# Performance work log

Hardware: AMD Instinct MI355X
Metric: run time of the kernel (lower is better)

The kernel has to match this reference:

```python
import jax, jax.numpy as jnp
from jax import lax
import numpy as np

B, T, I, H, OUT = 4096, 168, 4, 64, 12


def setup_inputs() -> dict:
    key = jax.random.key(0)
    ks = jax.random.split(key, 14)
    s = 0.05
    return {
        "x": jax.random.normal(ks[0], (B, T, I), dtype=jnp.float32),
        # LSTM layer 0 (PyTorch gate order: i, f, g, o)
        "Wih0": jax.random.normal(ks[1], (4 * H, I), dtype=jnp.float32) * s,
        "Whh0": jax.random.normal(ks[2], (4 * H, H), dtype=jnp.float32) * s,
        "bih0": jax.random.normal(ks[3], (4 * H,), dtype=jnp.float32) * s,
        "bhh0": jax.random.normal(ks[4], (4 * H,), dtype=jnp.float32) * s,
        # LSTM layer 1
        "Wih1": jax.random.normal(ks[5], (4 * H, H), dtype=jnp.float32) * s,
        "Whh1": jax.random.normal(ks[6], (4 * H, H), dtype=jnp.float32) * s,
        "bih1": jax.random.normal(ks[7], (4 * H,), dtype=jnp.float32) * s,
        "bhh1": jax.random.normal(ks[8], (4 * H,), dtype=jnp.float32) * s,
        # FC head: Linear(64,64) -> ReLU -> Linear(64,12)
        "W1": jax.random.normal(ks[9], (64, H), dtype=jnp.float32) * s,
        "b1": jax.random.normal(ks[10], (64,), dtype=jnp.float32) * s,
        "W2": jax.random.normal(ks[11], (OUT, 64), dtype=jnp.float32) * s,
        "b2": jax.random.normal(ks[12], (OUT,), dtype=jnp.float32) * s,
    }


def _lstm_layer(x, Wih, Whh, bih, bhh):
    # x: [B, T, in]; returns hidden sequence [B, T, H]
    Bsz = x.shape[0]
    Hd = Whh.shape[1]
    # Precompute input contribution for all timesteps: [B, T, 4H]
    xg = jnp.einsum('bti,gi->btg', x, Wih) + bih + bhh

    def step(carry, xg_t):
        h, c = carry
        g = xg_t + h @ Whh.T  # [B, 4H]
        i, f, gg, o = jnp.split(g, 4, axis=-1)
        i = jax.nn.sigmoid(i)
        f = jax.nn.sigmoid(f)
        gg = jnp.tanh(gg)
        o = jax.nn.sigmoid(o)
        c = f * c + i * gg
        h = o * jnp.tanh(c)
        return (h, c), h

    h0 = jnp.zeros((Bsz, Hd), x.dtype)
    (_, _), hs = lax.scan(step, (h0, h0), jnp.swapaxes(xg, 0, 1))  # hs: [T, B, H]
    return jnp.swapaxes(hs, 0, 1)


def reference(x, Wih0, Whh0, bih0, bhh0, Wih1, Whh1, bih1, bhh1, W1, b1, W2, b2):
    # Eval-mode forward: dropout layers are identity.
    h1 = _lstm_layer(x, Wih0, Whh0, bih0, bhh0)   # [B, T, H]
    h2 = _lstm_layer(h1, Wih1, Whh1, bih1, bhh1)  # [B, T, H]
    last = h2[:, -1, :]                            # [B, H]
    z = jax.nn.relu(last @ W1.T + b1)              # [B, 64]
    out = z @ W2.T + b2                            # [B, 12]
    return out.reshape(-1, 3, 4)
```

## Files before the change

### kernel.cpp

```cpp
#include <hip/hip_runtime.h>


typedef _Float16 h8 __attribute__((ext_vector_type(8)));
typedef _Float16 h4 __attribute__((ext_vector_type(4)));
typedef float f4 __attribute__((ext_vector_type(4)));

#define ROWB 208
#define HBUF (16 * ROWB)
#define H0_OFF 0
#define H1_OFF (2 * HBUF)
#define SMEM_TOTAL (4 * HBUF)

#define K1F 1.4426950408889634f
#define K2F 2.8853900817779268f

__device__ __forceinline__ float exp2_(float x) {
#if __has_builtin(__builtin_amdgcn_exp2f)
  return __builtin_amdgcn_exp2f(x);
#else
  float r; asm("v_exp_f32 %0, %1" : "=v"(r) : "v"(x)); return r;
#endif
}
__device__ __forceinline__ float rcp_(float x) {
#if __has_builtin(__builtin_amdgcn_rcpf)
  return __builtin_amdgcn_rcpf(x);
#else
  float r; asm("v_rcp_f32 %0, %1" : "=v"(r) : "v"(x)); return r;
#endif
}

__device__ __forceinline__ f4 mfma16(h8 a, h8 b, f4 c) {
  return __builtin_amdgcn_mfma_f32_16x16x32_f16(a, b, c, 0, 0, 0);
}

__device__ __forceinline__ h8 load_w8s(const float* __restrict__ p, float sc) {
  h8 r;
#pragma unroll
  for (int j = 0; j < 8; j++) r[j] = (_Float16)(p[j] * sc);
  return r;
}

__device__ __forceinline__ void lstm_act_s(float gi, float gf, float gg, float go,
                                           float& c, float& h) {
  float Ei = exp2_(-gi);
  float Ef = exp2_(-gf);
  float Eg = exp2_(gg);
  float Eo = exp2_(-go);
  float A = 1.f + Ei, B = 1.f + Ef, C = 1.f + Eg, D = 1.f + Eo;
  float AB = A * B, CD = C * D, BD = B * D;
  float R  = rcp_(AB * CD);
  float fv = (A * CD) * R;
  float ig = (BD * (Eg - 1.f)) * R;
  float ov = (AB * C) * R;
  c = fv * c + ig;
  float r2 = rcp_(exp2_(c * K2F) + 1.f);
  h = ov * (1.f - 2.f * r2);
}

extern "C" __global__ void __launch_bounds__(512, 2)
weather_lstm_mfma12(const float* __restrict__ x,
                    const float* __restrict__ Wih0, const float* __restrict__ Whh0,
                    const float* __restrict__ bih0, const float* __restrict__ bhh0,
                    const float* __restrict__ Wih1, const float* __restrict__ Whh1,
                    const float* __restrict__ bih1, const float* __restrict__ bhh1,
                    const float* __restrict__ W1, const float* __restrict__ b1,
                    const float* __restrict__ W2, const float* __restrict__ b2,
                    float* __restrict__ out)
{
  __shared__ __align__(16) unsigned char smem[SMEM_TOTAL];
  const int tid  = threadIdx.x;
  const int lane = tid & 63;
  const int w    = tid >> 6;
  const int col  = lane & 15;
  const int quad = lane >> 4;
  const int role = (w ^ (w >> 2)) & 1;
  const bool isL0 = (role == 0);
  const int adj  = (w >= 4) ? ((w & 1) ? -1 : 1) : 0;
  const int wl   = (w + adj) >> 1;
  const int u0   = wl * 16;
  const int uu   = u0 + quad * 4;
  const int sB   = blockIdx.x * 16;

  h8 wfrag[16];
  f4 bias[4];
#pragma unroll
  for (int g = 0; g < 4; ++g) {
    const float sc = (g == 2) ? K2F : K1F;
    const int r = g * 64 + u0 + col;
    if (isL0) {
#pragma unroll
      for (int f = 0; f < 2; ++f)
        wfrag[2 * g + f] = load_w8s(Whh0 + r * 64 + f * 32 + quad * 8, sc);
      h8 xw = {};
      if (quad == 0) {
#pragma unroll
        for (int j = 0; j < 4; ++j) xw[j] = (_Float16)(Wih0[r * 4 + j] * sc);
      }
      wfrag[8 + g] = xw;
#pragma unroll
      for (int j = 0; j < 4; ++j)
        bias[g][j] = (bih0[g * 64 + uu + j] + bhh0[g * 64 + uu + j]) * sc;
    } else {
#pragma unroll
      for (int f = 0; f < 2; ++f) {
        wfrag[2 * g + f]     = load_w8s(Wih1 + r * 64 + f * 32 + quad * 8, sc);
        wfrag[8 + 2 * g + f] = load_w8s(Whh1 + r * 64 + f * 32 + quad * 8, sc);
      }
#pragma unroll
      for (int j = 0; j < 4; ++j)
        bias[g][j] = (bih1[g * 64 + uu + j] + bhh1[g * 64 + uu + j]) * sc;
    }
  }

  for (int idx = tid; idx < SMEM_TOTAL / 4; idx += 512) ((int*)smem)[idx] = 0;
  __syncthreads();

  f4 xc = {};
  if (isL0 && quad == 0)
    xc = *(const f4*)(x + ((size_t)(sB + col) * 168 + 0) * 4);

  f4 acc[4];
  float cst[4] = {0.f, 0.f, 0.f, 0.f};
  float hl[4]  = {0.f, 0.f, 0.f, 0.f};
  const int bo = col * ROWB + quad * 16;
  const int wo = col * ROWB + uu * 2;

  for (int k = 0; k <= 169; ++k) {
    const int sl = k & 1, slp = sl ^ 1;

    if (isL0) {
      if (k <= 167) {
        const unsigned char* h0r = smem + H0_OFF + slp * HBUF;
        h8 b0  = *(const h8*)(h0r + bo);
        h8 b1v = *(const h8*)(h0r + bo + 64);
        h8 bx = {};
        if (quad == 0) {
#pragma unroll
          for (int j = 0; j < 4; ++j) bx[j] = (_Float16)xc[j];
        }
        {
          const int kn = (k < 167) ? k + 1 : k;
          f4 xn = xc;
          if (quad == 0)
            xn = *(const f4*)(x + ((size_t)(sB + col) * 168 + kn) * 4);
          xc = xn;
        }
#pragma unroll
        for (int g = 0; g < 4; ++g) acc[g] = mfma16(wfrag[2 * g], b0, bias[g]);
#pragma unroll
        for (int g = 0; g < 4; ++g) acc[g] = mfma16(wfrag[2 * g + 1], b1v, acc[g]);
#pragma unroll
        for (int g = 0; g < 4; ++g) acc[g] = mfma16(wfrag[8 + g], bx, acc[g]);
      }
    } else {
      if (k >= 2) {
        h4 hv;
#pragma unroll
        for (int a = 0; a < 4; ++a) {
          float ho;
          lstm_act_s(acc[0][a], acc[1][a], acc[2][a], acc[3][a], cst[a], ho);
          hl[a] = ho;
          hv[a] = (_Float16)ho;
        }
        *(h4*)(smem + H1_OFF + sl * HBUF + wo) = hv;
      }
    }
    __syncthreads();

    if (isL0) {
      if (k <= 167) {
        h4 hv;
#pragma unroll
        for (int a = 0; a < 4; ++a) {
          float ho;
          lstm_act_s(acc[0][a], acc[1][a], acc[2][a], acc[3][a], cst[a], ho);
          hv[a] = (_Float16)ho;
        }
        *(h4*)(smem + H0_OFF + sl * HBUF + wo) = hv;
      }
    } else {
      if (k >= 1 && k <= 168) {
        const unsigned char* h0r = smem + H0_OFF + slp * HBUF;
        const unsigned char* h1r = smem + H1_OFF + sl * HBUF;
        h8 b0  = *(const h8*)(h0r + bo);
        h8 b1v = *(const h8*)(h0r + bo + 64);
        h8 q0  = *(const h8*)(h1r + bo);
        h8 q1  = *(const h8*)(h1r + bo + 64);
#pragma unroll
        for (int g = 0; g < 4; ++g) acc[g] = mfma16(wfrag[2 * g], b0, bias[g]);
#pragma unroll
        for (int g = 0; g < 4; ++g) acc[g] = mfma16(wfrag[2 * g + 1], b1v, acc[g]);
#pragma unroll
        for (int g = 0; g < 4; ++g) acc[g] = mfma16(wfrag[8 + 2 * g], q0, acc[g]);
#pragma unroll
        for (int g = 0; g < 4; ++g) acc[g] = mfma16(wfrag[9 + 2 * g], q1, acc[g]);
      }
    }
    __syncthreads();
  }

  float* fh = (float*)smem;
  if (!isL0) {
    f4 hv; hv[0] = hl[0]; hv[1] = hl[1]; hv[2] = hl[2]; hv[3] = hl[3];
    *(f4*)(fh + col * 64 + uu) = hv;
  }
  __syncthreads();

  {
    const int u = tid & 63, g2 = tid >> 6;
    const float* w1r = W1 + u * 64;
    float* zl = (float*)(smem + 4096);
#pragma unroll
    for (int rep = 0; rep < 2; ++rep) {
      const int s2 = g2 + rep * 8;
      float za = b1[u];
      const float* f0 = fh + s2 * 64;
      for (int j = 0; j < 64; ++j) za += w1r[j] * f0[j];
      zl[s2 * 64 + u] = fmaxf(za, 0.f);
    }
  }
  __syncthreads();

  if (tid < 192) {
    const float* zl = (const float*)(smem + 4096);
    const int s2 = tid / 12, o = tid - s2 * 12;
    float a = b2[o];
    for (int j = 0; j < 64; ++j) a += W2[o * 64 + j] * zl[s2 * 64 + j];
    out[(sB + s2) * 12 + o] = a;
  }
}

extern "C" void kernel_launch(void* const* d_in, const int* in_sizes, int n_in,
                              void* d_out, int out_size, void* d_ws, size_t ws_size,
                              hipStream_t stream) {
  (void)in_sizes; (void)n_in; (void)d_ws; (void)ws_size; (void)out_size;
  const float* x    = (const float*)d_in[0];
  const float* Wih0 = (const float*)d_in[1];
  const float* Whh0 = (const float*)d_in[2];
  const float* bih0 = (const float*)d_in[3];
  const float* bhh0 = (const float*)d_in[4];
  const float* Wih1 = (const float*)d_in[5];
  const float* Whh1 = (const float*)d_in[6];
  const float* bih1 = (const float*)d_in[7];
  const float* bhh1 = (const float*)d_in[8];
  const float* W1   = (const float*)d_in[9];
  const float* b1   = (const float*)d_in[10];
  const float* W2   = (const float*)d_in[11];
  const float* b2   = (const float*)d_in[12];

  weather_lstm_mfma12<<<dim3(256), dim3(512), 0, stream>>>(
      x, Wih0, Whh0, bih0, bhh0, Wih1, Whh1, bih1, bhh1, W1, b1, W2, b2,
      (float*)d_out);
}
```

Baseline: 238.9 us.

## Merge layer-0 and layer-1 roles into each wave, one barrier per step

```diff
diff --git a/kernel.cpp b/kernel.cpp
--- a/kernel.cpp
+++ b/kernel.cpp
@@ -57,8 +57,8 @@
   h = ov * (1.f - 2.f * r2);
 }
 
-extern "C" __global__ void __launch_bounds__(512, 2)
-weather_lstm_mfma12(const float* __restrict__ x,
+extern "C" __global__ void __launch_bounds__(256, 1)
+weather_lstm_mfma13(const float* __restrict__ x,
                     const float* __restrict__ Wih0, const float* __restrict__ Whh0,
                     const float* __restrict__ bih0, const float* __restrict__ bhh0,
                     const float* __restrict__ Wih1, const float* __restrict__ Whh1,
@@ -73,134 +73,112 @@
   const int w    = tid >> 6;
   const int col  = lane & 15;
   const int quad = lane >> 4;
-  const int role = (w ^ (w >> 2)) & 1;
-  const bool isL0 = (role == 0);
-  const int adj  = (w >= 4) ? ((w & 1) ? -1 : 1) : 0;
-  const int wl   = (w + adj) >> 1;
-  const int u0   = wl * 16;
+  const int u0   = w * 16;
   const int uu   = u0 + quad * 4;
   const int sB   = blockIdx.x * 16;
 
-  h8 wfrag[16];
-  f4 bias[4];
+  h8 wW0[8], wX0[4], wI1[8], wH1[8];
+  f4 bias0[4], bias1[4];
 #pragma unroll
   for (int g = 0; g < 4; ++g) {
     const float sc = (g == 2) ? K2F : K1F;
     const int r = g * 64 + u0 + col;
-    if (isL0) {
-#pragma unroll
-      for (int f = 0; f < 2; ++f)
-        wfrag[2 * g + f] = load_w8s(Whh0 + r * 64 + f * 32 + quad * 8, sc);
-      h8 xw = {};
-      if (quad == 0) {
-#pragma unroll
-        for (int j = 0; j < 4; ++j) xw[j] = (_Float16)(Wih0[r * 4 + j] * sc);
-      }
-      wfrag[8 + g] = xw;
-#pragma unroll
-      for (int j = 0; j < 4; ++j)
-        bias[g][j] = (bih0[g * 64 + uu + j] + bhh0[g * 64 + uu + j]) * sc;
-    } else {
-#pragma unroll
-      for (int f = 0; f < 2; ++f) {
-        wfrag[2 * g + f]     = load_w8s(Wih1 + r * 64 + f * 32 + quad * 8, sc);
-        wfrag[8 + 2 * g + f] = load_w8s(Whh1 + r * 64 + f * 32 + quad * 8, sc);
-      }
-#pragma unroll
-      for (int j = 0; j < 4; ++j)
-        bias[g][j] = (bih1[g * 64 + uu + j] + bhh1[g * 64 + uu + j]) * sc;
-    }
-  }
-
-  for (int idx = tid; idx < SMEM_TOTAL / 4; idx += 512) ((int*)smem)[idx] = 0;
+#pragma unroll
+    for (int f = 0; f < 2; ++f) {
+      wW0[2 * g + f] = load_w8s(Whh0 + r * 64 + f * 32 + quad * 8, sc);
+      wI1[2 * g + f] = load_w8s(Wih1 + r * 64 + f * 32 + quad * 8, sc);
+      wH1[2 * g + f] = load_w8s(Whh1 + r * 64 + f * 32 + quad * 8, sc);
+    }
+    h8 xw = {};
+    if (quad == 0) {
+#pragma unroll
+      for (int j = 0; j < 4; ++j) xw[j] = (_Float16)(Wih0[r * 4 + j] * sc);
+    }
+    wX0[g] = xw;
+#pragma unroll
+    for (int j = 0; j < 4; ++j) {
+      bias0[g][j] = (bih0[g * 64 + uu + j] + bhh0[g * 64 + uu + j]) * sc;
+      bias1[g][j] = (bih1[g * 64 + uu + j] + bhh1[g * 64 + uu + j]) * sc;
+    }
+  }
+
+  for (int idx = tid; idx < SMEM_TOTAL / 4; idx += 256) ((int*)smem)[idx] = 0;
   __syncthreads();
 
   f4 xc = {};
-  if (isL0 && quad == 0)
+  if (quad == 0)
     xc = *(const f4*)(x + ((size_t)(sB + col) * 168 + 0) * 4);
 
-  f4 acc[4];
-  float cst[4] = {0.f, 0.f, 0.f, 0.f};
+  float c0s[4] = {0.f, 0.f, 0.f, 0.f};
+  float c1s[4] = {0.f, 0.f, 0.f, 0.f};
   float hl[4]  = {0.f, 0.f, 0.f, 0.f};
   const int bo = col * ROWB + quad * 16;
   const int wo = col * ROWB + uu * 2;
 
-  for (int k = 0; k <= 169; ++k) {
-    const int sl = k & 1, slp = sl ^ 1;
-
-    if (isL0) {
-      if (k <= 167) {
-        const unsigned char* h0r = smem + H0_OFF + slp * HBUF;
-        h8 b0  = *(const h8*)(h0r + bo);
-        h8 b1v = *(const h8*)(h0r + bo + 64);
-        h8 bx = {};
-        if (quad == 0) {
-#pragma unroll
-          for (int j = 0; j < 4; ++j) bx[j] = (_Float16)xc[j];
-        }
-        {
-          const int kn = (k < 167) ? k + 1 : k;
-          f4 xn = xc;
-          if (quad == 0)
-            xn = *(const f4*)(x + ((size_t)(sB + col) * 168 + kn) * 4);
-          xc = xn;
-        }
-#pragma unroll
-        for (int g = 0; g < 4; ++g) acc[g] = mfma16(wfrag[2 * g], b0, bias[g]);
-#pragma unroll
-        for (int g = 0; g < 4; ++g) acc[g] = mfma16(wfrag[2 * g + 1], b1v, acc[g]);
-#pragma unroll
-        for (int g = 0; g < 4; ++g) acc[g] = mfma16(wfrag[8 + g], bx, acc[g]);
+  for (int k = 0; k <= 168; ++k) {
+    const int kb = k & 1, kbn = kb ^ 1;
+    const unsigned char* h0r = smem + H0_OFF + kbn * HBUF;
+    unsigned char*       h0w = smem + H0_OFF + kb  * HBUF;
+    const unsigned char* h1r = smem + H1_OFF + kb  * HBUF;
+    unsigned char*       h1w = smem + H1_OFF + kbn * HBUF;
+
+    h8 b0  = *(const h8*)(h0r + bo);
+    h8 b1v = *(const h8*)(h0r + bo + 64);
+    h8 q0  = *(const h8*)(h1r + bo);
+    h8 q1  = *(const h8*)(h1r + bo + 64);
+    h8 bx = {};
+    if (quad == 0) {
+#pragma unroll
+      for (int j = 0; j < 4; ++j) bx[j] = (_Float16)xc[j];
+    }
+    {
+      const int kn = (k < 167) ? k + 1 : k;
+      f4 xn = xc;
+      if (quad == 0)
+        xn = *(const f4*)(x + ((size_t)(sB + col) * 168 + kn) * 4);
+      xc = xn;
+    }
+
+    f4 A[4], C[4];
+#pragma unroll
+    for (int g = 0; g < 4; ++g) A[g] = mfma16(wW0[2 * g], b0, bias0[g]);
+#pragma unroll
+    for (int g = 0; g < 4; ++g) C[g] = mfma16(wI1[2 * g], b0, bias1[g]);
+#pragma unroll
+    for (int g = 0; g < 4; ++g) A[g] = mfma16(wW0[2 * g + 1], b1v, A[g]);
+#pragma unroll
+    for (int g = 0; g < 4; ++g) C[g] = mfma16(wI1[2 * g + 1], b1v, C[g]);
+#pragma unroll
+    for (int g = 0; g < 4; ++g) A[g] = mfma16(wX0[g], bx, A[g]);
+#pragma unroll
+    for (int g = 0; g < 4; ++g) C[g] = mfma16(wH1[2 * g], q0, C[g]);
+#pragma unroll
+    for (int g = 0; g < 4; ++g) C[g] = mfma16(wH1[2 * g + 1], q1, C[g]);
+
+    if (k < 168) {
+      h4 hv;
+#pragma unroll
+      for (int a = 0; a < 4; ++a) {
+        float ho;
+        lstm_act_s(A[0][a], A[1][a], A[2][a], A[3][a], c0s[a], ho);
+        hv[a] = (_Float16)ho;
       }
-    } else {
-      if (k >= 2) {
-        h4 hv;
-#pragma unroll
-        for (int a = 0; a < 4; ++a) {
-          float ho;
-          lstm_act_s(acc[0][a], acc[1][a], acc[2][a], acc[3][a], cst[a], ho);
-          hl[a] = ho;
-          hv[a] = (_Float16)ho;
-        }
-        *(h4*)(smem + H1_OFF + sl * HBUF + wo) = hv;
+      *(h4*)(h0w + wo) = hv;
+    }
+    if (k >= 1) {
+      h4 hv;
+#pragma unroll
+      for (int a = 0; a < 4; ++a) {
+        lstm_act_s(C[0][a], C[1][a], C[2][a], C[3][a], c1s[a], hl[a]);
+        hv[a] = (_Float16)hl[a];
       }
+      *(h4*)(h1w + wo) = hv;
     }
     __syncthreads();
-
-    if (isL0) {
-      if (k <= 167) {
-        h4 hv;
-#pragma unroll
-        for (int a = 0; a < 4; ++a) {
-          float ho;
-          lstm_act_s(acc[0][a], acc[1][a], acc[2][a], acc[3][a], cst[a], ho);
-          hv[a] = (_Float16)ho;
-        }
-        *(h4*)(smem + H0_OFF + sl * HBUF + wo) = hv;
-      }
-    } else {
-      if (k >= 1 && k <= 168) {
-        const unsigned char* h0r = smem + H0_OFF + slp * HBUF;
-        const unsigned char* h1r = smem + H1_OFF + sl * HBUF;
-        h8 b0  = *(const h8*)(h0r + bo);
-        h8 b1v = *(const h8*)(h0r + bo + 64);
-        h8 q0  = *(const h8*)(h1r + bo);
-        h8 q1  = *(const h8*)(h1r + bo + 64);
-#pragma unroll
-        for (int g = 0; g < 4; ++g) acc[g] = mfma16(wfrag[2 * g], b0, bias[g]);
-#pragma unroll
-        for (int g = 0; g < 4; ++g) acc[g] = mfma16(wfrag[2 * g + 1], b1v, acc[g]);
-#pragma unroll
-        for (int g = 0; g < 4; ++g) acc[g] = mfma16(wfrag[8 + 2 * g], q0, acc[g]);
-#pragma unroll
-        for (int g = 0; g < 4; ++g) acc[g] = mfma16(wfrag[9 + 2 * g], q1, acc[g]);
-      }
-    }
-    __syncthreads();
   }
 
   float* fh = (float*)smem;
-  if (!isL0) {
+  {
     f4 hv; hv[0] = hl[0]; hv[1] = hl[1]; hv[2] = hl[2]; hv[3] = hl[3];
     *(f4*)(fh + col * 64 + uu) = hv;
   }
@@ -211,8 +189,8 @@
     const float* w1r = W1 + u * 64;
     float* zl = (float*)(smem + 4096);
 #pragma unroll
-    for (int rep = 0; rep < 2; ++rep) {
-      const int s2 = g2 + rep * 8;
+    for (int rep = 0; rep < 4; ++rep) {
+      const int s2 = g2 + rep * 4;
       float za = b1[u];
       const float* f0 = fh + s2 * 64;
       for (int j = 0; j < 64; ++j) za += w1r[j] * f0[j];
@@ -248,7 +226,7 @@
   const float* W2   = (const float*)d_in[11];
   const float* b2   = (const float*)d_in[12];
 
-  weather_lstm_mfma12<<<dim3(256), dim3(512), 0, stream>>>(
+  weather_lstm_mfma13<<<dim3(256), dim3(256), 0, stream>>>(
       x, Wih0, Whh0, bih0, bhh0, Wih1, Whh1, bih1, bhh1, W1, b1, W2, b2,
       (float*)d_out);
 }
```

Result: no change. 237.8 us (-0.5%).
